# Kernel tuning notes

Measured on AMD Instinct MI355X. Metric: run time of the kernel, lower is better.

The kernel has to match this reference:

```python
import jax, jax.numpy as jnp
import numpy as np

IN, OUT, LR = 4096, 4096, 64
TILE = (8, 8)

def setup_inputs() -> dict:
    key = jax.random.key(0)
    ks = jax.random.split(key, 8)
    return {
        "x": jax.random.normal(ks[0], (4, 2048, IN), dtype=jnp.float32),
        "frozen_random_matrix": jax.random.normal(ks[1], (OUT, IN), dtype=jnp.float16),
        "lowrank_first": jax.random.normal(ks[2], (LR, IN), dtype=jnp.float32) * 0.02,
        "lowrank_second": jax.random.normal(ks[3], (2 * OUT, LR), dtype=jnp.float32) * 0.02,
        "grid_scale": jax.random.normal(ks[4], (OUT // TILE[0], 1, IN // TILE[1], 1), dtype=jnp.float32),
        "grid_bias": jax.random.normal(ks[5], (OUT // TILE[0], 1, IN // TILE[1], 1), dtype=jnp.float32),
        "sparse_adapter": jnp.zeros((OUT, IN), dtype=jnp.float32),
        "scale": jax.random.normal(ks[6], (OUT,), dtype=jnp.float32),
        "bias": jax.random.normal(ks[7], (OUT,), dtype=jnp.float32),
    }

def reference(x, frozen_random_matrix, lowrank_first, lowrank_second,
              grid_scale, grid_bias, sparse_adapter, scale, bias):
    O, I = frozen_random_matrix.shape
    th, tw = TILE
    # Tiled affine reconstruction of the weight matrix, in fp16 (buffer dtype)
    m = frozen_random_matrix.reshape(O // th, th, I // tw, tw)
    m = grid_bias.astype(jnp.float16) + m * grid_scale.astype(jnp.float16)
    m = m.reshape(O, I) + sparse_adapter.astype(jnp.float16)
    # Dense GEMM in fp16, cast back to input dtype (mirrors input.to(matrix.dtype))
    baseline = jnp.matmul(x.astype(jnp.float16), m.T).astype(x.dtype)  # [B,S,O]
    # Low-rank adapter path
    hid = jnp.matmul(x, lowrank_first.T)                               # [B,S,LR]
    intercept = jnp.concatenate([scale, bias], axis=0)                 # [2*O]
    proj = jnp.matmul(hid, lowrank_second.T) + intercept               # [B,S,2*O]
    multiplicative, additive = proj[..., :O], proj[..., O:]
    return additive + multiplicative * baseline
```

## Files before the change

kernel.cpp:

```cpp
#include <hip/hip_runtime.h>
#include <stdint.h>

typedef _Float16 f16;
typedef unsigned short u16;
typedef __attribute__((ext_vector_type(8))) _Float16 h16x8;
typedef __attribute__((ext_vector_type(8))) unsigned short u16x8;
typedef __attribute__((ext_vector_type(4))) float f32x4;

#define NDIM  4096
#define KDIM  4096
#define LRDIM 64

__device__ __forceinline__ float bf2f(u16 b) {
  union { unsigned u; float f; } c; c.u = ((unsigned)b) << 16; return c.f;
}
__device__ __forceinline__ float h2f(u16 b) {
  union { u16 u; f16 h; } c; c.u = b; return (float)c.h;
}
__device__ __forceinline__ h16x8 pack8(float4 a, float4 b) {
  h16x8 w = { (f16)a.x, (f16)a.y, (f16)a.z, (f16)a.w,
              (f16)b.x, (f16)b.y, (f16)b.z, (f16)b.w };
  return w;
}

__device__ __forceinline__ void gll16(const void* g, void* l) {
  __builtin_amdgcn_global_load_lds(
      (const __attribute__((address_space(1))) void*)g,
      (__attribute__((address_space(3))) void*)l,
      16, 0, 0);
}

__device__ int frozen_mode(const void* frozen, int t) {
  const u16* fr = (const u16*)frozen;
  __shared__ int sE[256], sO[256];
  int ce = 0, co = 0;
  for (int j = 0; j < 8; ++j) {
    float ve = fabsf(bf2f(fr[t * 16 + 2 * j]));
    float vo = fabsf(bf2f(fr[t * 16 + 2 * j + 1]));
    if (ve >= 0.05f && ve <= 10.0f) ++ce;
    if (vo >= 0.05f && vo <= 10.0f) ++co;
  }
  sE[t] = ce; sO[t] = co;
  __syncthreads();
  for (int s = 128; s > 0; s >>= 1) {
    if (t < s) { sE[t] += sE[t + s]; sO[t] += sO[t + s]; }
    __syncthreads();
  }
  int te = sE[0], to = sO[0];
  __syncthreads();
  if (to > 1024) return (te > 1024) ? 1 : 2;
  return 0;
}

__device__ __forceinline__ h16x8 build_m8(
    const void* __restrict__ frozen, const float* __restrict__ gs,
    const float* __restrict__ gb, const float* __restrict__ sa,
    int o, int i0, int mode)
{
  size_t fo = (size_t)o * KDIM + i0;
  int gidx = (o >> 3) * 512 + (i0 >> 3);
  float gsf = gs[gidx], gbf = gb[gidx];
  float4 s0 = ((const float4*)(sa + fo))[0];
  float4 s1 = ((const float4*)(sa + fo))[1];
  float sv[8] = { s0.x, s0.y, s0.z, s0.w, s1.x, s1.y, s1.z, s1.w };
  float fv[8];
  if (mode == 2) {
    float4 q0 = ((const float4*)((const float*)frozen + fo))[0];
    float4 q1 = ((const float4*)((const float*)frozen + fo))[1];
    fv[0]=q0.x; fv[1]=q0.y; fv[2]=q0.z; fv[3]=q0.w;
    fv[4]=q1.x; fv[5]=q1.y; fv[6]=q1.z; fv[7]=q1.w;
  } else {
    u16x8 fb = *(const u16x8*)((const u16*)frozen + fo);
#pragma unroll
    for (int j = 0; j < 8; ++j) fv[j] = (mode == 1) ? bf2f(fb[j]) : h2f(fb[j]);
  }
  h16x8 w;
#pragma unroll
  for (int j = 0; j < 8; ++j) w[j] = (f16)(gbf + fv[j] * gsf + sv[j]);
  return w;
}

__global__ __launch_bounds__(256) void k9_build_m(
    const void* __restrict__ frozen, const float* __restrict__ gs,
    const float* __restrict__ gb, const float* __restrict__ sa,
    f16* __restrict__ mW)
{
  int mode = frozen_mode(frozen, threadIdx.x);
  int idx = blockIdx.x * 256 + threadIdx.x;
  int o  = idx >> 9;
  int ig = idx & 511;
  h16x8 w = build_m8(frozen, gs, gb, sa, o, ig * 8, mode);
  *(h16x8*)(mW + (size_t)o * KDIM + ig * 8) = w;
}

__global__ __launch_bounds__(256) void k9_cast_x(const float* __restrict__ x,
                                                 f16* __restrict__ xh)
{
  size_t idx = (size_t)blockIdx.x * 256 + threadIdx.x;
  const float4* xp = (const float4*)x + idx * 2;
  *(h16x8*)(xh + idx * 8) = pack8(xp[0], xp[1]);
}

__global__ __launch_bounds__(256) void k14_hid(const f16* __restrict__ xh,
                                               const float* __restrict__ L1,
                                               f16* __restrict__ hid)
{
  __shared__ f16 sA[2][32 * 32];
  __shared__ f16 sB[2][64 * 32];
  int t = threadIdx.x;
  int l = t & 63, wid = t >> 6;
  int wr = wid >> 1, wc = wid & 1;
  int brow = blockIdx.x * 32;
  int ar = t >> 2, ac8 = (t & 3) * 8;
  int brw = t >> 2, bc8 = (t & 3) * 8;

  f32x4 acc[2] = {};

  {
    if (t < 128)
      gll16(xh + (size_t)(brow + ar) * KDIM + ac8, &sA[0][ar * 32 + ac8]);
    const float* lp = L1 + (size_t)brw * KDIM + bc8;
    *(h16x8*)&sB[0][brw * 32 + bc8] = pack8(((const float4*)lp)[0], ((const float4*)lp)[1]);
  }

  int cur = 0;
  const int NT = KDIM / 32;
  for (int kt = 0; kt < NT; ++kt) {
    __syncthreads();
    bool pf = (kt + 1 < NT);
    h16x8 wb;
    if (pf) {
      int k0 = (kt + 1) * 32;
      if (t < 128)
        gll16(xh + (size_t)(brow + ar) * KDIM + k0 + ac8, &sA[cur ^ 1][ar * 32 + ac8]);
      const float* lp = L1 + (size_t)brw * KDIM + k0 + bc8;
      wb = pack8(((const float4*)lp)[0], ((const float4*)lp)[1]);
    }
    h16x8 aF, bF[2];
    aF = *(const h16x8*)&sA[cur][(wr * 16 + (l & 15)) * 32 + (l >> 4) * 8];
#pragma unroll
    for (int n = 0; n < 2; ++n)
      bF[n] = *(const h16x8*)&sB[cur][(wc * 32 + n * 16 + (l & 15)) * 32 + (l >> 4) * 8];
#pragma unroll
    for (int n = 0; n < 2; ++n)
      acc[n] = __builtin_amdgcn_mfma_f32_16x16x32_f16(aF, bF[n], acc[n], 0, 0, 0);
    if (pf)
      *(h16x8*)&sB[cur ^ 1][brw * 32 + bc8] = wb;
    cur ^= 1;
  }

#pragma unroll
  for (int n = 0; n < 2; ++n)
#pragma unroll
    for (int j = 0; j < 4; ++j) {
      int r = wr * 16 + ((l >> 4) << 2) + j;
      int c = wc * 32 + n * 16 + (l & 15);
      hid[(size_t)(brow + r) * LRDIM + c] = (f16)acc[n][j];
    }
}

__global__ __launch_bounds__(256, 3) void k17_main(
    const f16* __restrict__ xh, const f16* __restrict__ mW,
    const f16* __restrict__ hid, const float* __restrict__ L2,
    const float* __restrict__ scale, const float* __restrict__ bias,
    float* __restrict__ out)
{
  __shared__ f16 sA[2][128 * 32];
  __shared__ f16 sB[2][128 * 32];
  int t = threadIdx.x;
  int l = t & 63, wid = t >> 6;
  int wr = wid >> 1, wc = wid & 1;

  int wg = blockIdx.x;
  int xcd = wg & 7;
  int w = wg >> 3;
  int bm = xcd * 8 + (w & 7);
  int bn = w >> 3;
  int brow = bm * 128, bcol = bn * 128;

  int ur = t >> 2, uc8 = (t & 3) * 8;

  f32x4 acc[4][4] = {};

  gll16(xh + (size_t)(brow + ur) * KDIM + uc8,      &sA[0][ur * 32 + uc8]);
  gll16(xh + (size_t)(brow + ur + 64) * KDIM + uc8, &sA[0][(ur + 64) * 32 + uc8]);
  gll16(mW + (size_t)(bcol + ur) * KDIM + uc8,      &sB[0][ur * 32 + uc8]);
  gll16(mW + (size_t)(bcol + ur + 64) * KDIM + uc8, &sB[0][(ur + 64) * 32 + uc8]);

  int cur = 0;
  const int NT = KDIM / 32;
  for (int kt = 0; kt < NT; ++kt) {
    __syncthreads();
    if (kt + 1 < NT) {
      int k0 = (kt + 1) * 32;
      gll16(xh + (size_t)(brow + ur) * KDIM + k0 + uc8,      &sA[cur ^ 1][ur * 32 + uc8]);
      gll16(xh + (size_t)(brow + ur + 64) * KDIM + k0 + uc8, &sA[cur ^ 1][(ur + 64) * 32 + uc8]);
      gll16(mW + (size_t)(bcol + ur) * KDIM + k0 + uc8,      &sB[cur ^ 1][ur * 32 + uc8]);
      gll16(mW + (size_t)(bcol + ur + 64) * KDIM + k0 + uc8, &sB[cur ^ 1][(ur + 64) * 32 + uc8]);
    }
    h16x8 aF[4], bF[4];
#pragma unroll
    for (int m = 0; m < 4; ++m)
      aF[m] = *(const h16x8*)&sA[cur][(wr * 64 + m * 16 + (l & 15)) * 32 + (l >> 4) * 8];
#pragma unroll
    for (int n = 0; n < 4; ++n)
      bF[n] = *(const h16x8*)&sB[cur][(wc * 64 + n * 16 + (l & 15)) * 32 + (l >> 4) * 8];
#pragma unroll
    for (int m = 0; m < 4; ++m)
#pragma unroll
      for (int n = 0; n < 4; ++n)
        acc[m][n] = __builtin_amdgcn_mfma_f32_16x16x32_f16(aF[m], bF[n], acc[m][n], 0, 0, 0);
    cur ^= 1;
  }

  __syncthreads();
  f16* sH = &sA[0][0];
  f16* sL = &sB[0][0];

  for (int j = 0; j < 4; ++j) {
    int u = t + j * 256;
    int r = u >> 3, c8 = (u & 7) * 8;
    *(h16x8*)&sH[r * 64 + c8] =
        *(const h16x8*)(hid + (size_t)(brow + r) * LRDIM + c8);
    const float* lp = L2 + (size_t)(bcol + r) * LRDIM + c8;
    *(h16x8*)&sL[r * 64 + c8] = pack8(((const float4*)lp)[0], ((const float4*)lp)[1]);
  }
  __syncthreads();

  float sc[4], bi[4];
#pragma unroll
  for (int n = 0; n < 4; ++n) {
    int o = bcol + wc * 64 + n * 16 + (l & 15);
    sc[n] = scale[o];
    bi[n] = bias[o];
  }

  {
    h16x8 lB[4][2];
#pragma unroll
    for (int n = 0; n < 4; ++n)
#pragma unroll
      for (int kk = 0; kk < 2; ++kk)
        lB[n][kk] = *(const h16x8*)&sL[(wc * 64 + n * 16 + (l & 15)) * 64 + kk * 32 + (l >> 4) * 8];
#pragma unroll
    for (int m = 0; m < 4; ++m) {
      h16x8 hA0 = *(const h16x8*)&sH[(wr * 64 + m * 16 + (l & 15)) * 64 + (l >> 4) * 8];
      h16x8 hA1 = *(const h16x8*)&sH[(wr * 64 + m * 16 + (l & 15)) * 64 + 32 + (l >> 4) * 8];
      f32x4 mm[4];
#pragma unroll
      for (int n = 0; n < 4; ++n) {
        f32x4 mi = { sc[n], sc[n], sc[n], sc[n] };
        mm[n] = mi;
      }
#pragma unroll
      for (int n = 0; n < 4; ++n) {
        mm[n] = __builtin_amdgcn_mfma_f32_16x16x32_f16(hA0, lB[n][0], mm[n], 0, 0, 0);
        mm[n] = __builtin_amdgcn_mfma_f32_16x16x32_f16(hA1, lB[n][1], mm[n], 0, 0, 0);
      }
#pragma unroll
      for (int n = 0; n < 4; ++n)
        acc[m][n] *= mm[n];
    }
  }

  __syncthreads();
  for (int j = 0; j < 4; ++j) {
    int u = t + j * 256;
    int r = u >> 3, c8 = (u & 7) * 8;
    const float* lp = L2 + (size_t)(NDIM + bcol + r) * LRDIM + c8;
    *(h16x8*)&sL[r * 64 + c8] = pack8(((const float4*)lp)[0], ((const float4*)lp)[1]);
  }
  __syncthreads();

  {
    h16x8 lB[4][2];
#pragma unroll
    for (int n = 0; n < 4; ++n)
#pragma unroll
      for (int kk = 0; kk < 2; ++kk)
        lB[n][kk] = *(const h16x8*)&sL[(wc * 64 + n * 16 + (l & 15)) * 64 + kk * 32 + (l >> 4) * 8];
#pragma unroll
    for (int m = 0; m < 4; ++m) {
      h16x8 hA0 = *(const h16x8*)&sH[(wr * 64 + m * 16 + (l & 15)) * 64 + (l >> 4) * 8];
      h16x8 hA1 = *(const h16x8*)&sH[(wr * 64 + m * 16 + (l & 15)) * 64 + 32 + (l >> 4) * 8];
      f32x4 aa[4];
#pragma unroll
      for (int n = 0; n < 4; ++n) {
        f32x4 mi = { bi[n], bi[n], bi[n], bi[n] };
        aa[n] = mi;
      }
#pragma unroll
      for (int n = 0; n < 4; ++n) {
        aa[n] = __builtin_amdgcn_mfma_f32_16x16x32_f16(hA0, lB[n][0], aa[n], 0, 0, 0);
        aa[n] = __builtin_amdgcn_mfma_f32_16x16x32_f16(hA1, lB[n][1], aa[n], 0, 0, 0);
      }
      int rbase = brow + wr * 64 + m * 16 + ((l >> 4) << 2);
#pragma unroll
      for (int n = 0; n < 4; ++n) {
        int c = bcol + wc * 64 + n * 16 + (l & 15);
        f32x4 v = aa[n] + acc[m][n];
#pragma unroll
        for (int j = 0; j < 4; ++j)
          out[(size_t)(rbase + j) * NDIM + c] = v[j];
      }
    }
  }
}

extern "C" void kernel_launch(void* const* d_in, const int* in_sizes, int n_in,
                              void* d_out, int out_size, void* d_ws, size_t ws_size,
                              hipStream_t stream)
{
  const int SD[9] = {33554432,16777216,262144,524288,262144,262144,16777216,4096,4096};
  const int SA[9] = {4096,16777216,262144,262144,262144,524288,4096,16777216,33554432};
  bool dict = (n_in == 9), alph = (n_in == 9);
  if (n_in == 9) {
    for (int i = 0; i < 9; ++i) {
      if (in_sizes[i] != SD[i]) dict = false;
      if (in_sizes[i] != SA[i]) alph = false;
    }
  }
  if (!dict && !alph) {
    int ix = 0;
    for (int i = 0; i < n_in; ++i)
      if (in_sizes[i] == 33554432 || in_sizes[i] == 134217728) { ix = i; break; }
    dict = (ix == 0);
  }
  const float* x     = (const float*)d_in[dict ? 0 : 8];
  const void*  fr    =               d_in[1];
  const float* L1    = (const float*)d_in[dict ? 2 : 4];
  const float* L2    = (const float*)d_in[dict ? 3 : 5];
  const float* gs    = (const float*)d_in[dict ? 4 : 3];
  const float* gb    = (const float*)d_in[dict ? 5 : 2];
  const float* sa    = (const float*)d_in[dict ? 6 : 7];
  const float* scale = (const float*)d_in[dict ? 7 : 6];
  const float* bias  = (const float*)d_in[dict ? 8 : 0];
  float* out = (float*)d_out;

  const size_t MW_B = (size_t)NDIM * KDIM * 2;
  const size_t XH_B = (size_t)8192 * KDIM * 2;

  char* ws = (char*)d_ws;
  f16* mW  = (f16*)ws;
  f16* xh  = (f16*)(ws + MW_B);
  f16* hid = (f16*)(ws + MW_B + XH_B);

  k9_cast_x<<<dim3(16384), dim3(256), 0, stream>>>(x, xh);
  k9_build_m<<<dim3(8192), dim3(256), 0, stream>>>(fr, gs, gb, sa, mW);
  k14_hid<<<dim3(256), dim3(256), 0, stream>>>(xh, L1, hid);
  k17_main<<<dim3(2048), dim3(256), 0, stream>>>(
      xh, mW, hid, L2, scale, bias, out);
}
```

Measured before the change: 501.9 us.

## Enlarge main GEMM tile to 256x256 with triple-buffered LDS and interleaved loads

New measurement: 445.4 us. -11.3%, faster.

```diff
diff --git a/kernel.cpp b/kernel.cpp
--- a/kernel.cpp
+++ b/kernel.cpp
@@ -10,6 +10,9 @@
 #define NDIM  4096
 #define KDIM  4096
 #define LRDIM 64
+#define NTK   128
+
+#define MFMA16(a, b, c) __builtin_amdgcn_mfma_f32_16x16x32_f16((a), (b), (c), 0, 0, 0)
 
 __device__ __forceinline__ float bf2f(u16 b) {
   union { unsigned u; float f; } c; c.u = ((unsigned)b) << 16; return c.f;
@@ -143,7 +146,7 @@
       bF[n] = *(const h16x8*)&sB[cur][(wc * 32 + n * 16 + (l & 15)) * 32 + (l >> 4) * 8];
 #pragma unroll
     for (int n = 0; n < 2; ++n)
-      acc[n] = __builtin_amdgcn_mfma_f32_16x16x32_f16(aF, bF[n], acc[n], 0, 0, 0);
+      acc[n] = MFMA16(aF, bF[n], acc[n]);
     if (pf)
       *(h16x8*)&sB[cur ^ 1][brw * 32 + bc8] = wb;
     cur ^= 1;
@@ -159,78 +162,144 @@
     }
 }
 
-__global__ __launch_bounds__(256, 3) void k17_main(
+__global__ __launch_bounds__(512) void k18_main(
     const f16* __restrict__ xh, const f16* __restrict__ mW,
     const f16* __restrict__ hid, const float* __restrict__ L2,
     const float* __restrict__ scale, const float* __restrict__ bias,
     float* __restrict__ out)
 {
-  __shared__ f16 sA[2][128 * 32];
-  __shared__ f16 sB[2][128 * 32];
+  __shared__ f16 lds[3][16384];
+
   int t = threadIdx.x;
   int l = t & 63, wid = t >> 6;
-  int wr = wid >> 1, wc = wid & 1;
+  int wm = wid >> 2, wn = wid & 3;
 
   int wg = blockIdx.x;
-  int xcd = wg & 7;
-  int w = wg >> 3;
-  int bm = xcd * 8 + (w & 7);
-  int bn = w >> 3;
-  int brow = bm * 128, bcol = bn * 128;
-
-  int ur = t >> 2, uc8 = (t & 3) * 8;
-
-  f32x4 acc[4][4] = {};
-
-  gll16(xh + (size_t)(brow + ur) * KDIM + uc8,      &sA[0][ur * 32 + uc8]);
-  gll16(xh + (size_t)(brow + ur + 64) * KDIM + uc8, &sA[0][(ur + 64) * 32 + uc8]);
-  gll16(mW + (size_t)(bcol + ur) * KDIM + uc8,      &sB[0][ur * 32 + uc8]);
-  gll16(mW + (size_t)(bcol + ur + 64) * KDIM + uc8, &sB[0][(ur + 64) * 32 + uc8]);
-
-  int cur = 0;
-  const int NT = KDIM / 32;
-  for (int kt = 0; kt < NT; ++kt) {
-    __syncthreads();
-    if (kt + 1 < NT) {
-      int k0 = (kt + 1) * 32;
-      gll16(xh + (size_t)(brow + ur) * KDIM + k0 + uc8,      &sA[cur ^ 1][ur * 32 + uc8]);
-      gll16(xh + (size_t)(brow + ur + 64) * KDIM + k0 + uc8, &sA[cur ^ 1][(ur + 64) * 32 + uc8]);
-      gll16(mW + (size_t)(bcol + ur) * KDIM + k0 + uc8,      &sB[cur ^ 1][ur * 32 + uc8]);
-      gll16(mW + (size_t)(bcol + ur + 64) * KDIM + k0 + uc8, &sB[cur ^ 1][(ur + 64) * 32 + uc8]);
-    }
+  int xcd = wg & 7, w = wg >> 3;
+  int bm = xcd * 4 + (w & 3);
+  int bn = w >> 2;
+  int brow = bm * 256, bcol = bn * 256;
+
+  auto stage = [&](int q, int kt2, int buf) {
+    int u = q * 512 + t;
+    if (u < 1024) {
+      gll16(xh + (size_t)(brow + (u >> 2)) * KDIM + kt2 * 32 + (u & 3) * 8,
+            &lds[buf][u * 8]);
+    } else {
+      int v = u - 1024;
+      gll16(mW + (size_t)(bcol + (v >> 2)) * KDIM + kt2 * 32 + (v & 3) * 8,
+            &lds[buf][8192 + v * 8]);
+    }
+  };
+
+#pragma unroll
+  for (int q = 0; q < 4; ++q) stage(q, 0, 0);
+#pragma unroll
+  for (int q = 0; q < 4; ++q) stage(q, 1, 1);
+  asm volatile("s_waitcnt vmcnt(4)" ::: "memory");
+  __builtin_amdgcn_sched_barrier(0);
+  __builtin_amdgcn_s_barrier();
+
+  f32x4 acc[8][4] = {};
+
+  for (int kt = 0; kt < NTK; ++kt) {
+    const f16* A = &lds[kt % 3][0];
+    const f16* B = &lds[kt % 3][8192];
+    int sb = (kt + 2) % 3;
+    bool st = (kt + 2) < NTK;
+    int k2 = kt + 2;
+
+    int ar0 = (wm * 128 + (l & 15)) * 32 + (l >> 4) * 8;
+    int br0 = (wn * 64  + (l & 15)) * 32 + (l >> 4) * 8;
+
     h16x8 aF[4], bF[4];
-#pragma unroll
-    for (int m = 0; m < 4; ++m)
-      aF[m] = *(const h16x8*)&sA[cur][(wr * 64 + m * 16 + (l & 15)) * 32 + (l >> 4) * 8];
-#pragma unroll
-    for (int n = 0; n < 4; ++n)
-      bF[n] = *(const h16x8*)&sB[cur][(wc * 64 + n * 16 + (l & 15)) * 32 + (l >> 4) * 8];
-#pragma unroll
-    for (int m = 0; m < 4; ++m)
-#pragma unroll
-      for (int n = 0; n < 4; ++n)
-        acc[m][n] = __builtin_amdgcn_mfma_f32_16x16x32_f16(aF[m], bF[n], acc[m][n], 0, 0, 0);
-    cur ^= 1;
-  }
-
+
+#pragma unroll
+    for (int f = 0; f < 4; ++f) aF[f] = *(const h16x8*)&A[ar0 + f * 512];
+    bF[0] = *(const h16x8*)&B[br0];
+    bF[1] = *(const h16x8*)&B[br0 + 512];
+    if (st) stage(0, k2, sb);
+    __builtin_amdgcn_s_barrier();
+    __builtin_amdgcn_s_setprio(1);
+#pragma unroll
+    for (int f = 0; f < 4; ++f) {
+      acc[f][0] = MFMA16(aF[f], bF[0], acc[f][0]);
+      acc[f][1] = MFMA16(aF[f], bF[1], acc[f][1]);
+    }
+    __builtin_amdgcn_s_setprio(0);
+    __builtin_amdgcn_s_barrier();
+
+    bF[2] = *(const h16x8*)&B[br0 + 1024];
+    bF[3] = *(const h16x8*)&B[br0 + 1536];
+    if (st) stage(1, k2, sb);
+    __builtin_amdgcn_s_barrier();
+    __builtin_amdgcn_s_setprio(1);
+#pragma unroll
+    for (int f = 0; f < 4; ++f) {
+      acc[f][2] = MFMA16(aF[f], bF[2], acc[f][2]);
+      acc[f][3] = MFMA16(aF[f], bF[3], acc[f][3]);
+    }
+    __builtin_amdgcn_s_setprio(0);
+    __builtin_amdgcn_s_barrier();
+
+#pragma unroll
+    for (int f = 0; f < 4; ++f) aF[f] = *(const h16x8*)&A[ar0 + (f + 4) * 512];
+    if (st) stage(2, k2, sb);
+    __builtin_amdgcn_s_barrier();
+    __builtin_amdgcn_s_setprio(1);
+#pragma unroll
+    for (int f = 0; f < 4; ++f) {
+      acc[f + 4][0] = MFMA16(aF[f], bF[0], acc[f + 4][0]);
+      acc[f + 4][1] = MFMA16(aF[f], bF[1], acc[f + 4][1]);
+    }
+    __builtin_amdgcn_s_setprio(0);
+    __builtin_amdgcn_s_barrier();
+
+    if (st) stage(3, k2, sb);
+    if (kt < NTK - 2) {
+      asm volatile("s_waitcnt vmcnt(4)" ::: "memory");
+    } else {
+      asm volatile("s_waitcnt vmcnt(0)" ::: "memory");
+    }
+    __builtin_amdgcn_sched_barrier(0);
+    __builtin_amdgcn_s_barrier();
+    __builtin_amdgcn_s_setprio(1);
+#pragma unroll
+    for (int f = 0; f < 4; ++f) {
+      acc[f + 4][2] = MFMA16(aF[f], bF[2], acc[f + 4][2]);
+      acc[f + 4][3] = MFMA16(aF[f], bF[3], acc[f + 4][3]);
+    }
+    __builtin_amdgcn_s_setprio(0);
+    __builtin_amdgcn_s_barrier();
+  }
+
+  f16* sH  = &lds[0][0];
+  f16* sLm = &lds[1][0];
+  f16* sLa = &lds[2][0];
+
+#pragma unroll
+  for (int q = 0; q < 4; ++q) {
+    int u = q * 512 + t;
+    gll16(hid + (size_t)(brow + (u >> 3)) * LRDIM + (u & 7) * 8, &sH[u * 8]);
+  }
+#pragma unroll
+  for (int q = 0; q < 4; ++q) {
+    int u = q * 512 + t;
+    const float* lp = L2 + (size_t)(bcol + (u >> 3)) * LRDIM + (u & 7) * 8;
+    *(h16x8*)&sLm[u * 8] = pack8(((const float4*)lp)[0], ((const float4*)lp)[1]);
+  }
+#pragma unroll
+  for (int q = 0; q < 4; ++q) {
+    int u = q * 512 + t;
+    const float* lp = L2 + (size_t)(NDIM + bcol + (u >> 3)) * LRDIM + (u & 7) * 8;
+    *(h16x8*)&sLa[u * 8] = pack8(((const float4*)lp)[0], ((const float4*)lp)[1]);
+  }
   __syncthreads();
-  f16* sH = &sA[0][0];
-  f16* sL = &sB[0][0];
-
-  for (int j = 0; j < 4; ++j) {
-    int u = t + j * 256;
-    int r = u >> 3, c8 = (u & 7) * 8;
-    *(h16x8*)&sH[r * 64 + c8] =
-        *(const h16x8*)(hid + (size_t)(brow + r) * LRDIM + c8);
-    const float* lp = L2 + (size_t)(bcol + r) * LRDIM + c8;
-    *(h16x8*)&sL[r * 64 + c8] = pack8(((const float4*)lp)[0], ((const float4*)lp)[1]);
-  }
-  __syncthreads();
 
   float sc[4], bi[4];
 #pragma unroll
   for (int n = 0; n < 4; ++n) {
-    int o = bcol + wc * 64 + n * 16 + (l & 15);
+    int o = bcol + wn * 64 + n * 16 + (l & 15);
     sc[n] = scale[o];
     bi[n] = bias[o];
   }
@@ -241,11 +310,11 @@
     for (int n = 0; n < 4; ++n)
 #pragma unroll
       for (int kk = 0; kk < 2; ++kk)
-        lB[n][kk] = *(const h16x8*)&sL[(wc * 64 + n * 16 + (l & 15)) * 64 + kk * 32 + (l >> 4) * 8];
-#pragma unroll
-    for (int m = 0; m < 4; ++m) {
-      h16x8 hA0 = *(const h16x8*)&sH[(wr * 64 + m * 16 + (l & 15)) * 64 + (l >> 4) * 8];
-      h16x8 hA1 = *(const h16x8*)&sH[(wr * 64 + m * 16 + (l & 15)) * 64 + 32 + (l >> 4) * 8];
+        lB[n][kk] = *(const h16x8*)&sLm[(wn * 64 + n * 16 + (l & 15)) * 64 + kk * 32 + (l >> 4) * 8];
+#pragma unroll
+    for (int f = 0; f < 8; ++f) {
+      h16x8 h0 = *(const h16x8*)&sH[(wm * 128 + f * 16 + (l & 15)) * 64 + (l >> 4) * 8];
+      h16x8 h1 = *(const h16x8*)&sH[(wm * 128 + f * 16 + (l & 15)) * 64 + 32 + (l >> 4) * 8];
       f32x4 mm[4];
 #pragma unroll
       for (int n = 0; n < 4; ++n) {
@@ -254,23 +323,14 @@
       }
 #pragma unroll
       for (int n = 0; n < 4; ++n) {
-        mm[n] = __builtin_amdgcn_mfma_f32_16x16x32_f16(hA0, lB[n][0], mm[n], 0, 0, 0);
-        mm[n] = __builtin_amdgcn_mfma_f32_16x16x32_f16(hA1, lB[n][1], mm[n], 0, 0, 0);
+        mm[n] = MFMA16(h0, lB[n][0], mm[n]);
+        mm[n] = MFMA16(h1, lB[n][1], mm[n]);
       }
 #pragma unroll
       for (int n = 0; n < 4; ++n)
-        acc[m][n] *= mm[n];
-    }
-  }
-
-  __syncthreads();
-  for (int j = 0; j < 4; ++j) {
-    int u = t + j * 256;
-    int r = u >> 3, c8 = (u & 7) * 8;
-    const float* lp = L2 + (size_t)(NDIM + bcol + r) * LRDIM + c8;
-    *(h16x8*)&sL[r * 64 + c8] = pack8(((const float4*)lp)[0], ((const float4*)lp)[1]);
-  }
-  __syncthreads();
+        acc[f][n] *= mm[n];
+    }
+  }
 
   {
     h16x8 lB[4][2];
@@ -278,11 +338,11 @@
     for (int n = 0; n < 4; ++n)
 #pragma unroll
       for (int kk = 0; kk < 2; ++kk)
-        lB[n][kk] = *(const h16x8*)&sL[(wc * 64 + n * 16 + (l & 15)) * 64 + kk * 32 + (l >> 4) * 8];
-#pragma unroll
-    for (int m = 0; m < 4; ++m) {
-      h16x8 hA0 = *(const h16x8*)&sH[(wr * 64 + m * 16 + (l & 15)) * 64 + (l >> 4) * 8];
-      h16x8 hA1 = *(const h16x8*)&sH[(wr * 64 + m * 16 + (l & 15)) * 64 + 32 + (l >> 4) * 8];
+        lB[n][kk] = *(const h16x8*)&sLa[(wn * 64 + n * 16 + (l & 15)) * 64 + kk * 32 + (l >> 4) * 8];
+#pragma unroll
+    for (int f = 0; f < 8; ++f) {
+      h16x8 h0 = *(const h16x8*)&sH[(wm * 128 + f * 16 + (l & 15)) * 64 + (l >> 4) * 8];
+      h16x8 h1 = *(const h16x8*)&sH[(wm * 128 + f * 16 + (l & 15)) * 64 + 32 + (l >> 4) * 8];
       f32x4 aa[4];
 #pragma unroll
       for (int n = 0; n < 4; ++n) {
@@ -291,14 +351,14 @@
       }
 #pragma unroll
       for (int n = 0; n < 4; ++n) {
-        aa[n] = __builtin_amdgcn_mfma_f32_16x16x32_f16(hA0, lB[n][0], aa[n], 0, 0, 0);
-        aa[n] = __builtin_amdgcn_mfma_f32_16x16x32_f16(hA1, lB[n][1], aa[n], 0, 0, 0);
+        aa[n] = MFMA16(h0, lB[n][0], aa[n]);
+        aa[n] = MFMA16(h1, lB[n][1], aa[n]);
       }
-      int rbase = brow + wr * 64 + m * 16 + ((l >> 4) << 2);
+      int rbase = brow + wm * 128 + f * 16 + ((l >> 4) << 2);
 #pragma unroll
       for (int n = 0; n < 4; ++n) {
-        int c = bcol + wc * 64 + n * 16 + (l & 15);
-        f32x4 v = aa[n] + acc[m][n];
+        int c = bcol + wn * 64 + n * 16 + (l & 15);
+        f32x4 v = aa[n] + acc[f][n];
 #pragma unroll
         for (int j = 0; j < 4; ++j)
           out[(size_t)(rbase + j) * NDIM + c] = v[j];
@@ -348,6 +408,6 @@
   k9_cast_x<<<dim3(16384), dim3(256), 0, stream>>>(x, xh);
   k9_build_m<<<dim3(8192), dim3(256), 0, stream>>>(fr, gs, gb, sa, mW);
   k14_hid<<<dim3(256), dim3(256), 0, stream>>>(xh, L1, hid);
-  k17_main<<<dim3(2048), dim3(256), 0, stream>>>(
+  k18_main<<<dim3(512), dim3(512), 0, stream>>>(
       xh, mW, hid, L2, scale, bias, out);
 }
```
